# Optimization experiments

Hardware: AMD Instinct MI355X
Metric: run time of the kernel (lower is better)

Reference implementation:

```python
import jax, jax.numpy as jnp
import numpy as np

CHANNEL = 256
REDUCTION = 2
CI = CHANNEL // REDUCTION  # 128
B, H, W = 2, 80, 80


def setup_inputs() -> dict:
    key = jax.random.key(0)
    ks = jax.random.split(key, 9)
    s = 0.05
    return {
        "x": jax.random.normal(ks[0], (B, CHANNEL, H, W), jnp.float32),
        "g_w": jax.random.normal(ks[1], (CI, CHANNEL), jnp.float32) * s,
        "g_b": jax.random.normal(ks[2], (CI,), jnp.float32) * s,
        "theta_w": jax.random.normal(ks[3], (CI, CHANNEL), jnp.float32) * s,
        "theta_b": jax.random.normal(ks[4], (CI,), jnp.float32) * s,
        "phi_w": jax.random.normal(ks[5], (CI, CHANNEL), jnp.float32) * s,
        "phi_b": jax.random.normal(ks[6], (CI,), jnp.float32) * s,
        "W_w": jax.random.normal(ks[7], (CHANNEL, CI), jnp.float32) * s,
        "W_b": jax.random.normal(ks[8], (CHANNEL,), jnp.float32) * s,
    }


def _proj(x, w, b):
    # 1x1 conv == channel matmul: x [B,C,H,W], w [Co,C] -> [B,Co,H,W]
    return jnp.einsum('bchw,oc->bohw', x, w) + b[None, :, None, None]


def reference(x, g_w, g_b, theta_w, theta_b, phi_w, phi_b, W_w, W_b):
    b, c, h, w = x.shape
    n = h * w
    g_x = _proj(x, g_w, g_b).reshape(b, CI, n).transpose(0, 2, 1)        # [B,N,Ci]
    theta_x = _proj(x, theta_w, theta_b).reshape(b, CI, n).transpose(0, 2, 1)  # [B,N,Ci]
    phi_x = _proj(x, phi_w, phi_b).reshape(b, CI, n)                     # [B,Ci,N]
    f = jnp.einsum('bnc,bcm->bnm', theta_x, phi_x)                       # [B,N,N]
    # NOTE: original uses softmax over dim=1 (the theta/row axis), not dim=-1
    f_div_C = jax.nn.softmax(f, axis=1)
    y = jnp.einsum('bnm,bmc->bnc', f_div_C, g_x)                         # [B,N,Ci]
    y = y.transpose(0, 2, 1).reshape(b, CI, h, w)                        # [B,Ci,H,W]
    W_y = _proj(y, W_w, W_b)                                             # [B,C,H,W]
    return W_y + x
```

## Files before the change

kernel.cpp:

```cpp
#include <hip/hip_runtime.h>
#include <hip/hip_bf16.h>

#define NHW 6400
#define CIN 256
#define CIO 128
#define NB 2

typedef __bf16 bf16x8 __attribute__((ext_vector_type(8)));
typedef float f32x4 __attribute__((ext_vector_type(4)));

#define LOG2E 1.4426950408889634f
#define FSH (-20.0f * LOG2E)

__device__ __forceinline__ unsigned short f2bfu(float x) {
    union { float f; unsigned u; } a; a.f = x;
    unsigned r = (a.u + 0x7fffu + ((a.u >> 16) & 1u)) >> 16;
    return (unsigned short)r;
}
__device__ __forceinline__ float bfu2f(unsigned short v) {
    union { unsigned u; float f; } a; a.u = ((unsigned)v) << 16;
    return a.f;
}
__device__ __forceinline__ void splitbf(float v, unsigned short& h, unsigned short& l) {
    unsigned short hh = f2bfu(v);
    h = hh;
    l = f2bfu(v - bfu2f(hh));
}
__device__ __forceinline__ float pexp(float f) {
    return __builtin_amdgcn_exp2f(__builtin_fmaf(f, LOG2E, FSH));
}

#define MFMA(a, b, c) __builtin_amdgcn_mfma_f32_16x16x32_bf16((a), (b), (c), 0, 0, 0)

typedef const __attribute__((address_space(1))) unsigned gu32;
typedef __attribute__((address_space(3))) unsigned lu32;
__device__ __forceinline__ void gload16(const void* g, void* l) {
    __builtin_amdgcn_global_load_lds((gu32*)g, (lu32*)l, 16, 0, 0);
}

__device__ __forceinline__ void f_tile(
    const unsigned short* __restrict__ ph_hi, const unsigned short* __restrict__ ph_lo,
    size_t a0, size_t a1, const bf16x8* tBh, const bf16x8* tBl,
    f32x4& f0, f32x4& f1)
{
    const f32x4 z4 = {0.f, 0.f, 0.f, 0.f};
    f0 = z4; f1 = z4;
    #pragma unroll
    for (int kk = 0; kk < 4; ++kk) {
        bf16x8 Ah0 = *(const bf16x8*)(ph_hi + a0 + kk*32);
        bf16x8 Al0 = *(const bf16x8*)(ph_lo + a0 + kk*32);
        bf16x8 Ah1 = *(const bf16x8*)(ph_hi + a1 + kk*32);
        bf16x8 Al1 = *(const bf16x8*)(ph_lo + a1 + kk*32);
        f0 = MFMA(Ah0, tBh[kk], f0);
        f0 = MFMA(Ah0, tBl[kk], f0);
        f0 = MFMA(Al0, tBh[kk], f0);
        f1 = MFMA(Ah1, tBh[kk], f1);
        f1 = MFMA(Ah1, tBl[kk], f1);
        f1 = MFMA(Al1, tBh[kk], f1);
    }
}

__global__ __launch_bounds__(256) void k_zero(float* __restrict__ Zp) {
    const int i = blockIdx.x * 256 + threadIdx.x;
    if (i < NB * NHW) Zp[i] = 0.0f;
}
__global__ __launch_bounds__(256) void k_zeroy(float* __restrict__ yT) {
    const size_t i = (size_t)blockIdx.x * 256 + threadIdx.x;
    float4 z = {0.f, 0.f, 0.f, 0.f};
    *(float4*)&yT[i * 4] = z;
}

__global__ __launch_bounds__(256) void k_proj(
    const float* __restrict__ x,
    const float* __restrict__ gw, const float* __restrict__ gbias,
    const float* __restrict__ tw, const float* __restrict__ tbias,
    const float* __restrict__ pw, const float* __restrict__ pbias,
    unsigned short* __restrict__ th_hi, unsigned short* __restrict__ th_lo,
    unsigned short* __restrict__ ph_hi, unsigned short* __restrict__ ph_lo,
    float* __restrict__ g32)
{
    __shared__ float xT[16][260];
    const int n0 = blockIdx.x * 16;
    const int b  = blockIdx.y;
    const int t  = threadIdx.x;
    {
        const int nq = t & 3, cq = t >> 2;
        #pragma unroll
        for (int c0 = 0; c0 < 4; ++c0) {
            const int c = c0 * 64 + cq;
            float4 v = *(const float4*)&x[((size_t)b * CIN + c) * NHW + n0 + nq * 4];
            xT[nq*4+0][c] = v.x; xT[nq*4+1][c] = v.y;
            xT[nq*4+2][c] = v.z; xT[nq*4+3][c] = v.w;
        }
    }
    __syncthreads();
    const int ci = t & 127, nh = t >> 7;
    float aG[8], aT[8], aP[8];
    #pragma unroll
    for (int i = 0; i < 8; ++i) { aG[i]=0.f; aT[i]=0.f; aP[i]=0.f; }
    for (int c4 = 0; c4 < 64; ++c4) {
        float4 wg = *(const float4*)&gw[ci*CIN + c4*4];
        float4 wt = *(const float4*)&tw[ci*CIN + c4*4];
        float4 wp = *(const float4*)&pw[ci*CIN + c4*4];
        #pragma unroll
        for (int i = 0; i < 8; ++i) {
            float4 xv = *(const float4*)&xT[nh*8 + i][c4*4];
            aG[i] += wg.x*xv.x + wg.y*xv.y + wg.z*xv.z + wg.w*xv.w;
            aT[i] += wt.x*xv.x + wt.y*xv.y + wt.z*xv.z + wt.w*xv.w;
            aP[i] += wp.x*xv.x + wp.y*xv.y + wp.z*xv.z + wp.w*xv.w;
        }
    }
    const float bg = gbias[ci], bt = tbias[ci], bp = pbias[ci];
    #pragma unroll
    for (int i = 0; i < 8; ++i) {
        const size_t o = ((size_t)b * NHW + n0 + nh*8 + i) * CIO + ci;
        unsigned short h, l;
        splitbf(aT[i] + bt, h, l); th_hi[o] = h; th_lo[o] = l;
        splitbf(aP[i] + bp, h, l); ph_hi[o] = h; ph_lo[o] = l;
        g32[o] = aG[i] + bg;
    }
}

__global__ __launch_bounds__(256) void k_colsum(
    const unsigned short* __restrict__ ph_hi, const unsigned short* __restrict__ ph_lo,
    const unsigned short* __restrict__ th_hi, const unsigned short* __restrict__ th_lo,
    float* __restrict__ Zp)
{
    const int n0 = blockIdx.x * 16;
    const int mc = blockIdx.y * 1600;
    const int b  = blockIdx.z;
    const int w  = threadIdx.x >> 6;
    const int lane = threadIdx.x & 63;
    const int lm = lane & 15, kg = lane >> 4;
    bf16x8 tBh[4], tBl[4];
    {
        const size_t tb = ((size_t)b * NHW + n0 + lm) * CIO + kg * 8;
        #pragma unroll
        for (int kk = 0; kk < 4; ++kk) {
            tBh[kk] = *(const bf16x8*)(th_hi + tb + kk * 32);
            tBl[kk] = *(const bf16x8*)(th_lo + tb + kk * 32);
        }
    }
    for (int tt = w; tt < 50; tt += 4) {
        const int m0 = mc + tt * 32;
        const size_t a0 = ((size_t)b * NHW + m0 + lm) * CIO + kg * 8;
        const size_t a1 = a0 + (size_t)16 * CIO;
        f32x4 f0, f1;
        f_tile(ph_hi, ph_lo, a0, a1, tBh, tBl, f0, f1);
        #pragma unroll
        for (int j = 0; j < 4; ++j) {
            float v0 = pexp(f0[j]);
            v0 += __shfl_xor(v0, 1, 64); v0 += __shfl_xor(v0, 2, 64);
            v0 += __shfl_xor(v0, 4, 64); v0 += __shfl_xor(v0, 8, 64);
            float v1 = pexp(f1[j]);
            v1 += __shfl_xor(v1, 1, 64); v1 += __shfl_xor(v1, 2, 64);
            v1 += __shfl_xor(v1, 4, 64); v1 += __shfl_xor(v1, 8, 64);
            if ((lane & 15) == 0) {
                atomicAdd(&Zp[(size_t)b * NHW + m0 + kg*4 + j], v0);
                atomicAdd(&Zp[(size_t)b * NHW + m0 + 16 + kg*4 + j], v1);
            }
        }
    }
}

__global__ __launch_bounds__(256) void k_attn(
    const unsigned short* __restrict__ ph_hi, const unsigned short* __restrict__ ph_lo,
    const unsigned short* __restrict__ th_hi, const unsigned short* __restrict__ th_lo,
    const float* __restrict__ g32, const float* __restrict__ Zp,
    float* __restrict__ yT)
{
    __shared__ float gl[2][32][128];
    const int n0 = blockIdx.x * 32;
    const int mc = blockIdx.y * 1600;
    const int b  = blockIdx.z;
    const int w  = threadIdx.x >> 6;
    const int lane = threadIdx.x & 63;
    const int lm = lane & 15, kg = lane >> 4;
    const int c0 = w * 32 + kg * 8;
    bf16x8 tAh[4], tAl[4], tCh[4], tCl[4];
    {
        const size_t tba = ((size_t)b * NHW + n0 + lm) * CIO + kg * 8;
        const size_t tbc = tba + (size_t)16 * CIO;
        #pragma unroll
        for (int kk = 0; kk < 4; ++kk) {
            tAh[kk] = *(const bf16x8*)(th_hi + tba + kk * 32);
            tAl[kk] = *(const bf16x8*)(th_lo + tba + kk * 32);
            tCh[kk] = *(const bf16x8*)(th_hi + tbc + kk * 32);
            tCl[kk] = *(const bf16x8*)(th_lo + tbc + kk * 32);
        }
    }
    float acc0[8], acc1[8];
    #pragma unroll
    for (int i = 0; i < 8; ++i) { acc0[i] = 0.0f; acc1[i] = 0.0f; }

    const float* gbase = g32 + ((size_t)b * NHW + mc) * CIO;
    {
        #pragma unroll
        for (int q = 0; q < 4; ++q) {
            const int k = w * 4 + q;
            gload16(gbase + (size_t)k * 256 + lane * 4, &gl[0][2*k][0]);
        }
    }
    f32x4 f0a, f1a, f0c, f1c;
    {
        const size_t a0 = ((size_t)b * NHW + mc + lm) * CIO + kg * 8;
        const size_t a1 = a0 + (size_t)16 * CIO;
        f_tile(ph_hi, ph_lo, a0, a1, tAh, tAl, f0a, f1a);
        f_tile(ph_hi, ph_lo, a0, a1, tCh, tCl, f0c, f1c);
    }

    for (int t = 0; t < 50; ++t) {
        const int m0 = mc + t * 32;
        const float* zb = Zp + (size_t)b * NHW + m0;
        float rz[8];
        #pragma unroll
        for (int j = 0; j < 4; ++j) {
            rz[j]     = 1.0f / zb[kg*4 + j];
            rz[4 + j] = 1.0f / zb[16 + kg*4 + j];
        }
        float prega[8], pregc[8];
        #pragma unroll
        for (int j = 0; j < 4; ++j) {
            prega[j]     = pexp(f0a[j]) * rz[j];
            prega[4 + j] = pexp(f1a[j]) * rz[4 + j];
            pregc[j]     = pexp(f0c[j]) * rz[j];
            pregc[4 + j] = pexp(f1c[j]) * rz[4 + j];
        }
        __syncthreads();
        if (t < 49) {
            const float* gnext = gbase + (size_t)(t + 1) * 32 * CIO;
            #pragma unroll
            for (int q = 0; q < 4; ++q) {
                const int k = w * 4 + q;
                gload16(gnext + (size_t)k * 256 + lane * 4, &gl[(t+1)&1][2*k][0]);
            }
            const size_t a0 = ((size_t)b * NHW + m0 + 32 + lm) * CIO + kg * 8;
            const size_t a1 = a0 + (size_t)16 * CIO;
            f_tile(ph_hi, ph_lo, a0, a1, tAh, tAl, f0a, f1a);
            f_tile(ph_hi, ph_lo, a0, a1, tCh, tCl, f0c, f1c);
        }
        const float* gb = &gl[t & 1][0][0];
        #pragma unroll
        for (int mi = 0; mi < 32; ++mi) {
            const int kgp = (mi >> 2) & 3;
            const int jp  = (mi & 3) + ((mi >> 4) << 2);
            const int sl  = lm + 16 * kgp;
            const float psa = __shfl(prega[jp], sl, 64);
            const float psc = __shfl(pregc[jp], sl, 64);
            const float* gr = gb + mi * 128 + c0;
            float4 v0 = *(const float4*)(gr);
            float4 v1 = *(const float4*)(gr + 4);
            acc0[0] = __builtin_fmaf(psa, v0.x, acc0[0]);
            acc0[1] = __builtin_fmaf(psa, v0.y, acc0[1]);
            acc0[2] = __builtin_fmaf(psa, v0.z, acc0[2]);
            acc0[3] = __builtin_fmaf(psa, v0.w, acc0[3]);
            acc0[4] = __builtin_fmaf(psa, v1.x, acc0[4]);
            acc0[5] = __builtin_fmaf(psa, v1.y, acc0[5]);
            acc0[6] = __builtin_fmaf(psa, v1.z, acc0[6]);
            acc0[7] = __builtin_fmaf(psa, v1.w, acc0[7]);
            acc1[0] = __builtin_fmaf(psc, v0.x, acc1[0]);
            acc1[1] = __builtin_fmaf(psc, v0.y, acc1[1]);
            acc1[2] = __builtin_fmaf(psc, v0.z, acc1[2]);
            acc1[3] = __builtin_fmaf(psc, v0.w, acc1[3]);
            acc1[4] = __builtin_fmaf(psc, v1.x, acc1[4]);
            acc1[5] = __builtin_fmaf(psc, v1.y, acc1[5]);
            acc1[6] = __builtin_fmaf(psc, v1.z, acc1[6]);
            acc1[7] = __builtin_fmaf(psc, v1.w, acc1[7]);
        }
    }
    #pragma unroll
    for (int i = 0; i < 8; ++i) {
        atomicAdd(&yT[((size_t)b * CIO + c0 + i) * NHW + n0 + lm], acc0[i]);
        atomicAdd(&yT[((size_t)b * CIO + c0 + i) * NHW + n0 + 16 + lm], acc1[i]);
    }
}

__global__ __launch_bounds__(256) void k_wT(
    const float* __restrict__ Ww, float* __restrict__ WT)
{
    const int i = blockIdx.x * 256 + threadIdx.x;
    const int co = i >> 7, ci = i & 127;
    WT[(size_t)ci * CIN + co] = Ww[(size_t)co * CIO + ci];
}

__global__ __launch_bounds__(256) void k_out(
    const float* __restrict__ yT, const float* __restrict__ WT,
    const float* __restrict__ Wbias, const float* __restrict__ x,
    float* __restrict__ out)
{
    __shared__ float yl[128][20];
    const int n0 = blockIdx.x * 16;
    const int b  = blockIdx.y;
    const int t  = threadIdx.x;
    {
        const int c = t >> 1, nh = (t & 1) * 8;
        const float* yp = yT + ((size_t)b * CIO + c) * NHW + n0 + nh;
        float4 v0 = *(const float4*)(yp);
        float4 v1 = *(const float4*)(yp + 4);
        yl[c][nh+0] = v0.x; yl[c][nh+1] = v0.y; yl[c][nh+2] = v0.z; yl[c][nh+3] = v0.w;
        yl[c][nh+4] = v1.x; yl[c][nh+5] = v1.y; yl[c][nh+6] = v1.z; yl[c][nh+7] = v1.w;
    }
    __syncthreads();
    const int co = t;
    float acc[16];
    #pragma unroll
    for (int i = 0; i < 16; ++i) acc[i] = 0.0f;
    for (int ci = 0; ci < CIO; ++ci) {
        const float wv = WT[(size_t)ci * CIN + co];
        const float4 y0 = *(const float4*)&yl[ci][0];
        const float4 y1 = *(const float4*)&yl[ci][4];
        const float4 y2 = *(const float4*)&yl[ci][8];
        const float4 y3 = *(const float4*)&yl[ci][12];
        acc[0]  = __builtin_fmaf(wv, y0.x, acc[0]);
        acc[1]  = __builtin_fmaf(wv, y0.y, acc[1]);
        acc[2]  = __builtin_fmaf(wv, y0.z, acc[2]);
        acc[3]  = __builtin_fmaf(wv, y0.w, acc[3]);
        acc[4]  = __builtin_fmaf(wv, y1.x, acc[4]);
        acc[5]  = __builtin_fmaf(wv, y1.y, acc[5]);
        acc[6]  = __builtin_fmaf(wv, y1.z, acc[6]);
        acc[7]  = __builtin_fmaf(wv, y1.w, acc[7]);
        acc[8]  = __builtin_fmaf(wv, y2.x, acc[8]);
        acc[9]  = __builtin_fmaf(wv, y2.y, acc[9]);
        acc[10] = __builtin_fmaf(wv, y2.z, acc[10]);
        acc[11] = __builtin_fmaf(wv, y2.w, acc[11]);
        acc[12] = __builtin_fmaf(wv, y3.x, acc[12]);
        acc[13] = __builtin_fmaf(wv, y3.y, acc[13]);
        acc[14] = __builtin_fmaf(wv, y3.z, acc[14]);
        acc[15] = __builtin_fmaf(wv, y3.w, acc[15]);
    }
    const float wb = Wbias[co];
    const size_t ob = ((size_t)b * CIN + co) * NHW + n0;
    #pragma unroll
    for (int q = 0; q < 4; ++q) {
        float4 xv = *(const float4*)&x[ob + q*4];
        float4 ov;
        ov.x = acc[q*4+0] + xv.x + wb;
        ov.y = acc[q*4+1] + xv.y + wb;
        ov.z = acc[q*4+2] + xv.z + wb;
        ov.w = acc[q*4+3] + xv.w + wb;
        *(float4*)&out[ob + q*4] = ov;
    }
}

extern "C" void kernel_launch(void* const* d_in, const int* in_sizes, int n_in,
                              void* d_out, int out_size, void* d_ws, size_t ws_size,
                              hipStream_t stream)
{
    const float* x     = (const float*)d_in[0];
    const float* gw    = (const float*)d_in[1];
    const float* gbias = (const float*)d_in[2];
    const float* tw    = (const float*)d_in[3];
    const float* tbias = (const float*)d_in[4];
    const float* pw    = (const float*)d_in[5];
    const float* pbias = (const float*)d_in[6];
    const float* Ww    = (const float*)d_in[7];
    const float* Wbias = (const float*)d_in[8];

    char* ob = (char*)d_out;
    const size_t SZ = (size_t)NB * NHW * CIO * 2;
    unsigned short* th_hi = (unsigned short*)(ob);
    unsigned short* th_lo = (unsigned short*)(ob + SZ);
    unsigned short* ph_hi = (unsigned short*)(ob + 2*SZ);
    unsigned short* ph_lo = (unsigned short*)(ob + 3*SZ);

    char* ws = (char*)d_ws;
    const size_t SZF = (size_t)NB * NHW * CIO * 4;
    float* g32 = (float*)(ws);
    float* WT  = (float*)(ws);
    float* yT  = (float*)(ws + SZF);
    float* Zp  = (float*)(ws + 2*SZF);
    float* out = (float*)d_out;

    k_zero  <<<dim3(50),        256, 0, stream>>>(Zp);
    k_zeroy <<<dim3(1600),      256, 0, stream>>>(yT);
    k_proj  <<<dim3(400, 2),    256, 0, stream>>>(x, gw, gbias, tw, tbias, pw, pbias,
                                                  th_hi, th_lo, ph_hi, ph_lo, g32);
    k_colsum<<<dim3(400, 4, 2), 256, 0, stream>>>(ph_hi, ph_lo, th_hi, th_lo, Zp);
    k_attn  <<<dim3(200, 4, 2), 256, 0, stream>>>(ph_hi, ph_lo, th_hi, th_lo, g32, Zp, yT);
    k_wT    <<<dim3(128),       256, 0, stream>>>(Ww, WT);
    k_out   <<<dim3(400, 2),    256, 0, stream>>>(yT, WT, Wbias, x, out);
}
```

Before: 1.860 ms.

## Restructure attention kernel with per-wave g staging and smaller m tiles

The attention kernel now processes 16 key columns per step instead of 32 and splits the m range into 8 chunks, doubling the grid. Each wave stages only its own 32-channel slice of g in a private double buffer. Ordering is enforced with vmcnt waits instead of block-wide __syncthreads, which removes block-level barriers from the inner loop. The cost is more blocks doing atomic adds into yT and less reuse of each staged tile.

```diff
diff --git a/kernel.cpp b/kernel.cpp
--- a/kernel.cpp
+++ b/kernel.cpp
@@ -60,6 +60,22 @@
     }
 }
 
+__device__ __forceinline__ void f16c(
+    const unsigned short* __restrict__ ph_hi, const unsigned short* __restrict__ ph_lo,
+    size_t a0, const bf16x8* tBh, const bf16x8* tBl, f32x4& f0)
+{
+    const f32x4 z4 = {0.f, 0.f, 0.f, 0.f};
+    f0 = z4;
+    #pragma unroll
+    for (int kk = 0; kk < 4; ++kk) {
+        bf16x8 Ah0 = *(const bf16x8*)(ph_hi + a0 + kk*32);
+        bf16x8 Al0 = *(const bf16x8*)(ph_lo + a0 + kk*32);
+        f0 = MFMA(Ah0, tBh[kk], f0);
+        f0 = MFMA(Ah0, tBl[kk], f0);
+        f0 = MFMA(Al0, tBh[kk], f0);
+    }
+}
+
 __global__ __launch_bounds__(256) void k_zero(float* __restrict__ Zp) {
     const int i = blockIdx.x * 256 + threadIdx.x;
     if (i < NB * NHW) Zp[i] = 0.0f;
@@ -169,14 +185,14 @@
     const float* __restrict__ g32, const float* __restrict__ Zp,
     float* __restrict__ yT)
 {
-    __shared__ float gl[2][32][128];
+    __shared__ float gl[4][2][8][32];
     const int n0 = blockIdx.x * 32;
-    const int mc = blockIdx.y * 1600;
+    const int mc = blockIdx.y * 800;
     const int b  = blockIdx.z;
     const int w  = threadIdx.x >> 6;
     const int lane = threadIdx.x & 63;
     const int lm = lane & 15, kg = lane >> 4;
-    const int c0 = w * 32 + kg * 8;
+    const int cw = w * 32;
     bf16x8 tAh[4], tAl[4], tCh[4], tCl[4];
     {
         const size_t tba = ((size_t)b * NHW + n0 + lm) * CIO + kg * 8;
@@ -193,61 +209,38 @@
     #pragma unroll
     for (int i = 0; i < 8; ++i) { acc0[i] = 0.0f; acc1[i] = 0.0f; }
 
-    const float* gbase = g32 + ((size_t)b * NHW + mc) * CIO;
-    {
-        #pragma unroll
-        for (int q = 0; q < 4; ++q) {
-            const int k = w * 4 + q;
-            gload16(gbase + (size_t)k * 256 + lane * 4, &gl[0][2*k][0]);
-        }
-    }
-    f32x4 f0a, f1a, f0c, f1c;
+    const float* gsrc = g32 + ((size_t)b * NHW + mc + (lane >> 3)) * CIO
+                            + cw + (lane & 7) * 4;
+    char* bufw = (char*)&gl[w][0][0][0];
+    #define STAGE(k) gload16(gsrc + (size_t)(k) * 8 * CIO, bufw + ((k) & 1) * 1024)
+
+    STAGE(0);
+    STAGE(1);
+    f32x4 f0a, f0c;
     {
         const size_t a0 = ((size_t)b * NHW + mc + lm) * CIO + kg * 8;
-        const size_t a1 = a0 + (size_t)16 * CIO;
-        f_tile(ph_hi, ph_lo, a0, a1, tAh, tAl, f0a, f1a);
-        f_tile(ph_hi, ph_lo, a0, a1, tCh, tCl, f0c, f1c);
+        f16c(ph_hi, ph_lo, a0, tAh, tAl, f0a);
+        f16c(ph_hi, ph_lo, a0, tCh, tCl, f0c);
     }
 
     for (int t = 0; t < 50; ++t) {
-        const int m0 = mc + t * 32;
+        const int m0 = mc + t * 16;
         const float* zb = Zp + (size_t)b * NHW + m0;
-        float rz[8];
+        float prega[4], pregc[4];
         #pragma unroll
         for (int j = 0; j < 4; ++j) {
-            rz[j]     = 1.0f / zb[kg*4 + j];
-            rz[4 + j] = 1.0f / zb[16 + kg*4 + j];
-        }
-        float prega[8], pregc[8];
-        #pragma unroll
-        for (int j = 0; j < 4; ++j) {
-            prega[j]     = pexp(f0a[j]) * rz[j];
-            prega[4 + j] = pexp(f1a[j]) * rz[4 + j];
-            pregc[j]     = pexp(f0c[j]) * rz[j];
-            pregc[4 + j] = pexp(f1c[j]) * rz[4 + j];
-        }
-        __syncthreads();
-        if (t < 49) {
-            const float* gnext = gbase + (size_t)(t + 1) * 32 * CIO;
-            #pragma unroll
-            for (int q = 0; q < 4; ++q) {
-                const int k = w * 4 + q;
-                gload16(gnext + (size_t)k * 256 + lane * 4, &gl[(t+1)&1][2*k][0]);
-            }
-            const size_t a0 = ((size_t)b * NHW + m0 + 32 + lm) * CIO + kg * 8;
-            const size_t a1 = a0 + (size_t)16 * CIO;
-            f_tile(ph_hi, ph_lo, a0, a1, tAh, tAl, f0a, f1a);
-            f_tile(ph_hi, ph_lo, a0, a1, tCh, tCl, f0c, f1c);
-        }
-        const float* gb = &gl[t & 1][0][0];
-        #pragma unroll
-        for (int mi = 0; mi < 32; ++mi) {
-            const int kgp = (mi >> 2) & 3;
-            const int jp  = (mi & 3) + ((mi >> 4) << 2);
-            const int sl  = lm + 16 * kgp;
-            const float psa = __shfl(prega[jp], sl, 64);
-            const float psc = __shfl(pregc[jp], sl, 64);
-            const float* gr = gb + mi * 128 + c0;
+            const float r = 1.0f / zb[kg*4 + j];
+            prega[j] = pexp(f0a[j]) * r;
+            pregc[j] = pexp(f0c[j]) * r;
+        }
+        asm volatile("s_waitcnt vmcnt(1)" ::: "memory");
+        __builtin_amdgcn_sched_barrier(0);
+        #pragma unroll
+        for (int mi = 0; mi < 8; ++mi) {
+            const int kgp = mi >> 2, jp = mi & 3;
+            const float psa = __shfl(prega[jp], lm + 16*kgp, 64);
+            const float psc = __shfl(pregc[jp], lm + 16*kgp, 64);
+            const float* gr = &gl[w][0][mi][kg * 8];
             float4 v0 = *(const float4*)(gr);
             float4 v1 = *(const float4*)(gr + 4);
             acc0[0] = __builtin_fmaf(psa, v0.x, acc0[0]);
@@ -267,11 +260,51 @@
             acc1[6] = __builtin_fmaf(psc, v1.z, acc1[6]);
             acc1[7] = __builtin_fmaf(psc, v1.w, acc1[7]);
         }
-    }
+        if (t < 49) {
+            STAGE(2*t + 2);
+            asm volatile("s_waitcnt vmcnt(1)" ::: "memory");
+        } else {
+            asm volatile("s_waitcnt vmcnt(0)" ::: "memory");
+        }
+        __builtin_amdgcn_sched_barrier(0);
+        #pragma unroll
+        for (int mi = 0; mi < 8; ++mi) {
+            const int mig = 8 + mi;
+            const int kgp = mig >> 2, jp = mig & 3;
+            const float psa = __shfl(prega[jp], lm + 16*kgp, 64);
+            const float psc = __shfl(pregc[jp], lm + 16*kgp, 64);
+            const float* gr = &gl[w][1][mi][kg * 8];
+            float4 v0 = *(const float4*)(gr);
+            float4 v1 = *(const float4*)(gr + 4);
+            acc0[0] = __builtin_fmaf(psa, v0.x, acc0[0]);
+            acc0[1] = __builtin_fmaf(psa, v0.y, acc0[1]);
+            acc0[2] = __builtin_fmaf(psa, v0.z, acc0[2]);
+            acc0[3] = __builtin_fmaf(psa, v0.w, acc0[3]);
+            acc0[4] = __builtin_fmaf(psa, v1.x, acc0[4]);
+            acc0[5] = __builtin_fmaf(psa, v1.y, acc0[5]);
+            acc0[6] = __builtin_fmaf(psa, v1.z, acc0[6]);
+            acc0[7] = __builtin_fmaf(psa, v1.w, acc0[7]);
+            acc1[0] = __builtin_fmaf(psc, v0.x, acc1[0]);
+            acc1[1] = __builtin_fmaf(psc, v0.y, acc1[1]);
+            acc1[2] = __builtin_fmaf(psc, v0.z, acc1[2]);
+            acc1[3] = __builtin_fmaf(psc, v0.w, acc1[3]);
+            acc1[4] = __builtin_fmaf(psc, v1.x, acc1[4]);
+            acc1[5] = __builtin_fmaf(psc, v1.y, acc1[5]);
+            acc1[6] = __builtin_fmaf(psc, v1.z, acc1[6]);
+            acc1[7] = __builtin_fmaf(psc, v1.w, acc1[7]);
+        }
+        if (t < 49) {
+            STAGE(2*t + 3);
+            const size_t a0 = ((size_t)b * NHW + m0 + 16 + lm) * CIO + kg * 8;
+            f16c(ph_hi, ph_lo, a0, tAh, tAl, f0a);
+            f16c(ph_hi, ph_lo, a0, tCh, tCl, f0c);
+        }
+    }
+    #undef STAGE
     #pragma unroll
     for (int i = 0; i < 8; ++i) {
-        atomicAdd(&yT[((size_t)b * CIO + c0 + i) * NHW + n0 + lm], acc0[i]);
-        atomicAdd(&yT[((size_t)b * CIO + c0 + i) * NHW + n0 + 16 + lm], acc1[i]);
+        atomicAdd(&yT[((size_t)b * CIO + cw + kg*8 + i) * NHW + n0 + lm], acc0[i]);
+        atomicAdd(&yT[((size_t)b * CIO + cw + kg*8 + i) * NHW + n0 + 16 + lm], acc1[i]);
     }
 }
 
@@ -376,7 +409,7 @@
     k_proj  <<<dim3(400, 2),    256, 0, stream>>>(x, gw, gbias, tw, tbias, pw, pbias,
                                                   th_hi, th_lo, ph_hi, ph_lo, g32);
     k_colsum<<<dim3(400, 4, 2), 256, 0, stream>>>(ph_hi, ph_lo, th_hi, th_lo, Zp);
-    k_attn  <<<dim3(200, 4, 2), 256, 0, stream>>>(ph_hi, ph_lo, th_hi, th_lo, g32, Zp, yT);
+    k_attn  <<<dim3(200, 8, 2), 256, 0, stream>>>(ph_hi, ph_lo, th_hi, th_lo, g32, Zp, yT);
     k_wT    <<<dim3(128),       256, 0, stream>>>(Ww, WT);
     k_out   <<<dim3(400, 2),    256, 0, stream>>>(yT, WT, Wbias, x, out);
 }
```

Result: no change. 1.853 ms (-0.4%).
